# Kernel optimization log

Measured on AMD Instinct MI355X. Metric: run time of the kernel, lower is better.

The kernel has to match this reference:

```python
import jax, jax.numpy as jnp
import numpy as np

B, ISIZE, N, OSIZE = 2048, 512, 2048, 128
TC = 1.0 / 10.0  # dt/tau
PX = 0.5


def setup_inputs() -> dict:
    key = jax.random.key(0)
    ks = jax.random.split(key, 16)
    s = 0.01
    return {
        "x": jax.random.normal(ks[0], (B, ISIZE), jnp.float32),
        "h0_in": jax.random.normal(ks[1], (B, N), jnp.float32),
        "h1_in": jax.random.normal(ks[2], (B, N), jnp.float32),
        "h2_in": jax.random.normal(ks[3], (B, N), jnp.float32),
        "i_to_h0": s * jax.random.normal(ks[4], (ISIZE, N), jnp.float32),
        "h0_w": s * jax.random.normal(ks[5], (N, N), jnp.float32),
        "h0_b": s * jax.random.uniform(ks[6], (N,), jnp.float32),
        "h0_to_h1": s * jax.random.normal(ks[7], (N, N), jnp.float32),
        "h1_w": s * jax.random.normal(ks[8], (N, N), jnp.float32),
        "h1_b": s * jax.random.uniform(ks[9], (N,), jnp.float32),
        "h1_to_h2": s * jax.random.normal(ks[10], (N, N), jnp.float32),
        "h2_w": s * jax.random.normal(ks[11], (N, N), jnp.float32),
        "h2_b": s * jax.random.uniform(ks[12], (N,), jnp.float32),
        "w_out": s * jax.random.normal(ks[13], (N, OSIZE), jnp.float32),
        # Bernoulli(px) sparsity masks (non-trainable buffers in the original)
        "m01": (jax.random.uniform(ks[14], (N, N)) < PX).astype(jnp.float32),
        "m12": (jax.random.uniform(ks[15], (N, N)) < PX).astype(jnp.float32),
    }


def reference(x, h0_in, h1_in, h2_in, i_to_h0, h0_w, h0_b, h0_to_h1,
              h1_w, h1_b, h1_to_h2, h2_w, h2_b, w_out, m01, m12):
    tc = TC
    # zero-diagonal mask applied to every recurrent weight (no self-connections)
    diag = 1.0 - jnp.eye(N, dtype=h0_w.dtype)
    # replicate_ashok=True: feedforward weights are sparsified by Bernoulli masks
    h01 = h0_to_h1 * m01
    h12 = h1_to_h2 * m12

    # layer 0: input drive + masked recurrence + leaky integration
    h0 = h0_in * (1.0 - tc) + jax.nn.relu(
        x @ i_to_h0 + h0_in @ (h0_w * diag) + h0_b) * tc
    # layer 1
    h1 = h1_in * (1.0 - tc) + jax.nn.relu(
        h0 @ h01 + h1_in @ (h1_w * diag) + h1_b) * tc
    # layer 2
    h2 = h2_in * (1.0 - tc) + jax.nn.relu(
        h1 @ h12 + h2_in @ (h2_w * diag) + h2_b) * tc

    out = h2 @ w_out  # Linear without bias (replicate_ashok=True)
    return (h0, h1, h2, out)
```

## Files before the change

kernel.cpp:

```cpp
#include <hip/hip_runtime.h>
#include <hip/hip_bf16.h>
#include <stdint.h>

typedef __bf16 bf16;
typedef __bf16 bf16x8 __attribute__((ext_vector_type(8)));
typedef float f32x4 __attribute__((ext_vector_type(4)));

#define BB   2048
#define ISZ  512
#define NN   2048
#define OSZ  128

struct PackD { const float* src; bf16* dst; int W, ld, off, n8; };
struct TD    { const float* src; const float* msk; bf16* dst;
               int Ncols, ld_dst, k_off, mode, ntx, start; };
struct PAll  { PackD p[4]; TD d[7]; int packBlocks; };

__global__ __launch_bounds__(256) void prep_all_k(PAll a) {
  if ((int)blockIdx.x < a.packBlocks) {
    int idx = blockIdx.x * 256 + threadIdx.x;
    PackD d = a.p[0]; int base = 0;
#pragma unroll
    for (int i = 1; i < 4; ++i) if (idx >= a.p[i - 1].n8) { d = a.p[i]; base = a.p[i - 1].n8; }
    if (idx >= d.n8) return;
    int e = (idx - base) * 8;
    int m = e / d.W;
    int c = e - m * d.W;
    const float4 v0 = *reinterpret_cast<const float4*>(d.src + e);
    const float4 v1 = *reinterpret_cast<const float4*>(d.src + e + 4);
    bf16x8 o;
    o[0] = (bf16)v0.x; o[1] = (bf16)v0.y; o[2] = (bf16)v0.z; o[3] = (bf16)v0.w;
    o[4] = (bf16)v1.x; o[5] = (bf16)v1.y; o[6] = (bf16)v1.z; o[7] = (bf16)v1.w;
    *reinterpret_cast<bf16x8*>(d.dst + (size_t)m * d.ld + d.off + c) = o;
    return;
  }
  int bid = blockIdx.x - a.packBlocks;
  TD d = a.d[0];
#pragma unroll
  for (int i = 1; i < 7; ++i) if (bid >= a.d[i].start) d = a.d[i];
  int local = bid - d.start;
  int k0 = (local % d.ntx) * 32;
  int n0 = (local / d.ntx) * 32;
  __shared__ float t[32][33];
  const int tx = threadIdx.x & 31, ty = threadIdx.x >> 5;
#pragma unroll
  for (int i = 0; i < 4; ++i) {
    int k = k0 + ty + i * 8;
    float v = d.src[(size_t)k * d.Ncols + n0 + tx];
    if (d.mode == 1 && k == (n0 + tx)) v = 0.f;
    if (d.mode == 2) v *= d.msk[(size_t)k * d.Ncols + n0 + tx];
    t[ty + i * 8][tx] = v;
  }
  __syncthreads();
#pragma unroll
  for (int i = 0; i < 4; ++i) {
    int n = n0 + ty + i * 8;
    d.dst[(size_t)n * d.ld_dst + d.k_off + k0 + tx] = (bf16)t[tx][ty + i * 8];
  }
}

struct GP {
  const bf16* A; const bf16* B;
  int K, lda, ldb;
  const float* hin; const float* bias; const float* radd;
  float* outf; int ld_out;
  bf16* nxt; int ld_nxt;
  int epi;
};

__device__ __forceinline__ void gload16(const bf16* g, bf16* l) {
  __builtin_amdgcn_global_load_lds(
      (const __attribute__((address_space(1))) void*)g,
      (__attribute__((address_space(3))) void*)l, 16, 0, 0);
}

__device__ __forceinline__ void epilogue_store(const GP& p, int row, int col, float v) {
  size_t oidx = (size_t)row * p.ld_out + col;
  if (p.epi == 0) {
    float pre = v + p.bias[col];
    if (p.radd) pre += p.radd[oidx];
    float h = p.hin[oidx] * 0.9f + fmaxf(pre, 0.f) * 0.1f;
    p.outf[oidx] = h;
    p.nxt[(size_t)row * p.ld_nxt + col] = (bf16)h;
  } else {
    p.outf[oidx] = v;
  }
}

template<int BM, int BN>
__device__ __forceinline__ void gemm_body8(const GP p) {
  constexpr int BK = 32;
  constexpr int WM = BM / 2, WN = BN / 4;
  constexpr int FM = WM / 16, FN = WN / 16;
  __shared__ bf16 As[2][BM][BK];
  __shared__ bf16 Bs[2][BN][BK];
  const int tid  = threadIdx.x;
  const int lane = tid & 63;
  const int wave = tid >> 6;
  const int gx = gridDim.x, nwg = gx * gridDim.y;
  const int lid = blockIdx.x + gx * blockIdx.y;
  const int q = nwg >> 3;
  const int swz = (lid & 7) * q + (lid >> 3);
  const int m0 = (swz / gx) * BM, n0 = (swz % gx) * BN;
  const int wm0 = (wave >> 2) * WM, wn0 = (wave & 3) * WN;
  const int srow = lane >> 2;
  const int scolE = (((lane & 3) ^ ((lane >> 3) & 3)) * 8);
  const int frow = lane & 15;
  const int rcolE = (((lane >> 4) ^ ((frow >> 1) & 3)) * 8);

  f32x4 acc[FM][FN];
#pragma unroll
  for (int i = 0; i < FM; ++i)
#pragma unroll
    for (int j = 0; j < FN; ++j)
#pragma unroll
      for (int r = 0; r < 4; ++r) acc[i][j][r] = 0.f;

  auto stage = [&](int buf, int t) {
    const int k0 = t * BK;
#pragma unroll
    for (int c = wave; c < BM / 16; c += 8) {
      const bf16* g = p.A + (size_t)(m0 + c * 16 + srow) * p.lda + k0 + scolE;
      gload16(g, &As[buf][0][0] + c * 512);
    }
#pragma unroll
    for (int c = wave; c < BN / 16; c += 8) {
      const bf16* g = p.B + (size_t)(n0 + c * 16 + srow) * p.ldb + k0 + scolE;
      gload16(g, &Bs[buf][0][0] + c * 512);
    }
  };

  const int nt = p.K / BK;
  stage(0, 0);
  __syncthreads();
  int cur = 0;
  for (int t = 0; t < nt; ++t) {
    if (t + 1 < nt) stage(cur ^ 1, t + 1);
    bf16x8 af[FM], bfrag[FN];
#pragma unroll
    for (int i = 0; i < FM; ++i)
      af[i] = *reinterpret_cast<const bf16x8*>(&As[cur][wm0 + i * 16 + frow][rcolE]);
#pragma unroll
    for (int j = 0; j < FN; ++j)
      bfrag[j] = *reinterpret_cast<const bf16x8*>(&Bs[cur][wn0 + j * 16 + frow][rcolE]);
#pragma unroll
    for (int i = 0; i < FM; ++i)
#pragma unroll
      for (int j = 0; j < FN; ++j)
        acc[i][j] = __builtin_amdgcn_mfma_f32_16x16x32_bf16(af[i], bfrag[j], acc[i][j], 0, 0, 0);
    __syncthreads();
    cur ^= 1;
  }

#pragma unroll
  for (int i = 0; i < FM; ++i)
#pragma unroll
    for (int j = 0; j < FN; ++j)
#pragma unroll
      for (int r = 0; r < 4; ++r)
        epilogue_store(p, m0 + wm0 + i * 16 + (lane >> 4) * 4 + r,
                       n0 + wn0 + j * 16 + (lane & 15), acc[i][j][r]);
}

__global__ __launch_bounds__(512) void k_tri(GP p0, GP p1, GP p2) {
  GP p;
  if (blockIdx.z == 0) p = p0;
  else if (blockIdx.z == 1) p = p1;
  else p = p2;
  gemm_body8<128, 128>(p);
}

__global__ __launch_bounds__(512) void k_split(GP p0, GP p1) {
  gemm_body8<128, 128>(blockIdx.z == 0 ? p0 : p1);
}

__global__ __launch_bounds__(512) void k_out(GP p) { gemm_body8<32, 64>(p); }

__global__ __launch_bounds__(256) void k_epi(const float* __restrict__ P0,
                                             const float* __restrict__ P1,
                                             const float* __restrict__ radd,
                                             const float* __restrict__ hin,
                                             const float* __restrict__ bias,
                                             float* __restrict__ outf,
                                             bf16* __restrict__ nxt) {
  int e = (blockIdx.x * 256 + threadIdx.x) * 8;
  int colb = e & (NN - 1);
  const float4 a0 = *reinterpret_cast<const float4*>(P0 + e);
  const float4 a1 = *reinterpret_cast<const float4*>(P0 + e + 4);
  const float4 b0 = *reinterpret_cast<const float4*>(P1 + e);
  const float4 b1 = *reinterpret_cast<const float4*>(P1 + e + 4);
  const float4 r0 = *reinterpret_cast<const float4*>(radd + e);
  const float4 r1 = *reinterpret_cast<const float4*>(radd + e + 4);
  const float4 h0 = *reinterpret_cast<const float4*>(hin + e);
  const float4 h1 = *reinterpret_cast<const float4*>(hin + e + 4);
  const float4 c0 = *reinterpret_cast<const float4*>(bias + colb);
  const float4 c1 = *reinterpret_cast<const float4*>(bias + colb + 4);
  float pa[8] = {a0.x, a0.y, a0.z, a0.w, a1.x, a1.y, a1.z, a1.w};
  float pb[8] = {b0.x, b0.y, b0.z, b0.w, b1.x, b1.y, b1.z, b1.w};
  float pr[8] = {r0.x, r0.y, r0.z, r0.w, r1.x, r1.y, r1.z, r1.w};
  float ph[8] = {h0.x, h0.y, h0.z, h0.w, h1.x, h1.y, h1.z, h1.w};
  float pc[8] = {c0.x, c0.y, c0.z, c0.w, c1.x, c1.y, c1.z, c1.w};
  float4 o0, o1;
  bf16x8 nb;
#pragma unroll
  for (int j = 0; j < 8; ++j) {
    float pre = pa[j] + pb[j] + pr[j] + pc[j];
    float h = ph[j] * 0.9f + fmaxf(pre, 0.f) * 0.1f;
    (j < 4 ? (&o0.x)[j] : (&o1.x)[j - 4]) = h;
    nb[j] = (bf16)h;
  }
  *reinterpret_cast<float4*>(outf + e) = o0;
  *reinterpret_cast<float4*>(outf + e + 4) = o1;
  *reinterpret_cast<bf16x8*>(nxt + e) = nb;
}

extern "C" void kernel_launch(void* const* d_in, const int* in_sizes, int n_in,
                              void* d_out, int out_size, void* d_ws, size_t ws_size,
                              hipStream_t stream) {
  const float* x        = (const float*)d_in[0];
  const float* h0_in    = (const float*)d_in[1];
  const float* h1_in    = (const float*)d_in[2];
  const float* h2_in    = (const float*)d_in[3];
  const float* i_to_h0  = (const float*)d_in[4];
  const float* h0_w     = (const float*)d_in[5];
  const float* h0_b     = (const float*)d_in[6];
  const float* h0_to_h1 = (const float*)d_in[7];
  const float* h1_w     = (const float*)d_in[8];
  const float* h1_b     = (const float*)d_in[9];
  const float* h1_to_h2 = (const float*)d_in[10];
  const float* h2_w     = (const float*)d_in[11];
  const float* h2_b     = (const float*)d_in[12];
  const float* w_out    = (const float*)d_in[13];
  const float* m01      = (const float*)d_in[14];
  const float* m12      = (const float*)d_in[15];
  float* out = (float*)d_out;

  uint8_t* ws = (uint8_t*)d_ws;
  constexpr size_t OFF_A0  = 0;
  constexpr size_t OFF_W0  = OFF_A0 + 10485760;
  constexpr size_t OFF_W1R = OFF_W0 + 10485760;
  constexpr size_t OFF_W2R = OFF_W1R + 8388608;
  constexpr size_t OFF_W01 = OFF_W2R + 8388608;
  constexpr size_t OFF_W12 = OFF_W01 + 8388608;
  constexpr size_t OFF_WO  = OFF_W12 + 8388608;
  constexpr size_t OFF_AR1 = OFF_WO + 524288;
  constexpr size_t OFF_AR2 = OFF_AR1 + 8388608;
  constexpr size_t OFF_AH0 = OFF_AR2 + 8388608;
  constexpr size_t WS_NEED = OFF_AH0 + 8388608;
  if (ws_size < WS_NEED) return;

  bf16* A0  = (bf16*)(ws + OFF_A0);
  bf16* Wt0 = (bf16*)(ws + OFF_W0);
  bf16* W1r = (bf16*)(ws + OFF_W1R);
  bf16* W2r = (bf16*)(ws + OFF_W2R);
  bf16* W01 = (bf16*)(ws + OFF_W01);
  bf16* W12 = (bf16*)(ws + OFF_W12);
  bf16* WtO = (bf16*)(ws + OFF_WO);
  bf16* Ar1 = (bf16*)(ws + OFF_AR1);
  bf16* Ar2 = (bf16*)(ws + OFF_AR2);
  bf16* Ah0 = (bf16*)(ws + OFF_AH0);
  bf16* Ah1 = Ar1;
  bf16* Ah2 = Ar2;
  float* P0 = (float*)(ws + 0);
  float* P1 = (float*)(ws + 16777216);

  float* o_h0  = out;
  float* o_h1  = out + (size_t)BB * NN;
  float* o_h2  = out + (size_t)2 * BB * NN;
  float* o_out = out + (size_t)3 * BB * NN;

  PAll pa;
  int n8a = BB * ISZ / 8;
  int n8b = n8a + BB * NN / 8;
  int n8c = n8b + BB * NN / 8;
  int n8d = n8c + BB * NN / 8;
  pa.p[0] = {x,     A0,  ISZ, ISZ + NN, 0,   n8a};
  pa.p[1] = {h0_in, A0,  NN,  ISZ + NN, ISZ, n8b};
  pa.p[2] = {h1_in, Ar1, NN,  NN,       0,   n8c};
  pa.p[3] = {h2_in, Ar2, NN,  NN,       0,   n8d};
  pa.packBlocks = (n8d + 255) / 256;
  int s0 = 0;
  pa.d[0] = {i_to_h0,  nullptr, Wt0, NN,  ISZ + NN, 0,   0, ISZ / 32, s0}; s0 += (ISZ / 32) * (NN / 32);
  pa.d[1] = {h0_w,     nullptr, Wt0, NN,  ISZ + NN, ISZ, 1, NN / 32,  s0}; s0 += (NN / 32) * (NN / 32);
  pa.d[2] = {h1_w,     nullptr, W1r, NN,  NN,       0,   1, NN / 32,  s0}; s0 += (NN / 32) * (NN / 32);
  pa.d[3] = {h2_w,     nullptr, W2r, NN,  NN,       0,   1, NN / 32,  s0}; s0 += (NN / 32) * (NN / 32);
  pa.d[4] = {h0_to_h1, m01,     W01, NN,  NN,       0,   2, NN / 32,  s0}; s0 += (NN / 32) * (NN / 32);
  pa.d[5] = {h1_to_h2, m12,     W12, NN,  NN,       0,   2, NN / 32,  s0}; s0 += (NN / 32) * (NN / 32);
  pa.d[6] = {w_out,    nullptr, WtO, OSZ, NN,       0,   0, NN / 32,  s0}; s0 += (NN / 32) * (OSZ / 32);
  prep_all_k<<<pa.packBlocks + s0, 256, 0, stream>>>(pa);

  GP pS0{A0,  Wt0, ISZ + NN, ISZ + NN, ISZ + NN, h0_in, h0_b, nullptr,
         o_h0, NN, Ah0, NN, 0};
  GP pR1{Ar1, W1r, NN, NN, NN, nullptr, nullptr, nullptr, o_h1, NN, nullptr, 0, 1};
  GP pR2{Ar2, W2r, NN, NN, NN, nullptr, nullptr, nullptr, o_h2, NN, nullptr, 0, 1};
  k_tri<<<dim3(NN / 128, BB / 128, 3), 512, 0, stream>>>(pS0, pR1, pR2);

  GP pG1a{Ah0,          W01,          NN / 2, NN, NN, nullptr, nullptr, nullptr, P0, NN, nullptr, 0, 1};
  GP pG1b{Ah0 + NN / 2, W01 + NN / 2, NN / 2, NN, NN, nullptr, nullptr, nullptr, P1, NN, nullptr, 0, 1};
  k_split<<<dim3(NN / 128, BB / 128, 2), 512, 0, stream>>>(pG1a, pG1b);
  k_epi<<<BB * NN / 2048, 256, 0, stream>>>(P0, P1, o_h1, h1_in, h1_b, o_h1, Ah1);

  GP pG2a{Ah1,          W12,          NN / 2, NN, NN, nullptr, nullptr, nullptr, P0, NN, nullptr, 0, 1};
  GP pG2b{Ah1 + NN / 2, W12 + NN / 2, NN / 2, NN, NN, nullptr, nullptr, nullptr, P1, NN, nullptr, 0, 1};
  k_split<<<dim3(NN / 128, BB / 128, 2), 512, 0, stream>>>(pG2a, pG2b);
  k_epi<<<BB * NN / 2048, 256, 0, stream>>>(P0, P1, o_h2, h2_in, h2_b, o_h2, Ah2);

  GP pO{Ah2, WtO, NN, NN, NN, nullptr, nullptr, nullptr, o_out, OSZ, nullptr, 0, 1};
  k_out<<<dim3(OSZ / 64, BB / 32), 512, 0, stream>>>(pO);
}
```

Measured before the change: 257.6 us.

## Use intra-block split-K GEMM with BK=64 for the big 128x128 GEMMs

Adds a new GEMM body for the large 128x128 tile kernels. It uses a 64-wide K step and splits the 8 waves into two K-halves that each compute a 64x64 sub-tile per wave, then reduces the two partial accumulators through LDS before the fused epilogue. The aim is to halve the number of barriers per unit of K and raise MFMA work per LDS load, at the cost of more LDS, more registers and an extra reduction step. The small output GEMM loses its grouped tile swizzle and now uses plain block indexing.

```diff
diff --git a/kernel.cpp b/kernel.cpp
--- a/kernel.cpp
+++ b/kernel.cpp
@@ -87,6 +87,103 @@
   }
 }
 
+__device__ __forceinline__ void gemm_ks(const GP p) {
+  __shared__ __align__(16) bf16 sm[2][2][128][64];
+  const int lane = threadIdx.x & 63;
+  const int wave = threadIdx.x >> 6;
+  const int ks = wave >> 2;
+  const int sp = wave & 3;
+  const int gx = gridDim.x, nwg = gx * gridDim.y;
+  const int lid = blockIdx.x + gx * blockIdx.y;
+  const int q = nwg >> 3;
+  const int swz = (lid & 7) * q + (lid >> 3);
+  const int m0 = (swz / gx) * 128, n0 = (swz % gx) * 128;
+  const int wm0 = (sp >> 1) * 64, wn0 = (sp & 1) * 64;
+  const int srow = lane >> 3;
+  const int scol = ((lane & 7) ^ srow) * 8;
+  const int frow = lane & 15;
+  const int rcol = (((ks << 2) + (lane >> 4)) ^ (frow & 7)) * 8;
+
+  f32x4 acc[4][4];
+#pragma unroll
+  for (int i = 0; i < 4; ++i)
+#pragma unroll
+    for (int j = 0; j < 4; ++j)
+#pragma unroll
+      for (int r = 0; r < 4; ++r) acc[i][j][r] = 0.f;
+
+  auto stage = [&](int buf, int t) {
+    const int k0 = t * 64;
+#pragma unroll
+    for (int h = 0; h < 2; ++h) {
+      const int c = wave + h * 8;
+      gload16(p.A + (size_t)(m0 + c * 8 + srow) * p.lda + k0 + scol,
+              &sm[buf][0][0][0] + c * 512);
+      gload16(p.B + (size_t)(n0 + c * 8 + srow) * p.ldb + k0 + scol,
+              &sm[buf][1][0][0] + c * 512);
+    }
+  };
+
+  const int nt = p.K / 64;
+  stage(0, 0);
+  int cur = 0;
+  for (int t = 0; t < nt; ++t) {
+    if (t + 1 < nt) {
+      stage(cur ^ 1, t + 1);
+      asm volatile("s_waitcnt vmcnt(4)" ::: "memory");
+    } else {
+      asm volatile("s_waitcnt vmcnt(0)" ::: "memory");
+    }
+    __builtin_amdgcn_s_barrier();
+
+    bf16x8 af[4], bf_[4];
+#pragma unroll
+    for (int i = 0; i < 4; ++i)
+      af[i] = *reinterpret_cast<const bf16x8*>(&sm[cur][0][wm0 + i * 16 + frow][rcol]);
+#pragma unroll
+    for (int j = 0; j < 4; ++j)
+      bf_[j] = *reinterpret_cast<const bf16x8*>(&sm[cur][1][wn0 + j * 16 + frow][rcol]);
+#pragma unroll
+    for (int i = 0; i < 4; ++i)
+#pragma unroll
+      for (int j = 0; j < 4; ++j)
+        acc[i][j] = __builtin_amdgcn_mfma_f32_16x16x32_bf16(af[i], bf_[j], acc[i][j], 0, 0, 0);
+
+    if (t + 1 < nt) {
+      asm volatile("s_waitcnt lgkmcnt(0)" ::: "memory");
+      __builtin_amdgcn_s_barrier();
+    }
+    cur ^= 1;
+  }
+
+  asm volatile("s_waitcnt lgkmcnt(0)" ::: "memory");
+  __builtin_amdgcn_s_barrier();
+  float* red = (float*)&sm[0][0][0][0];
+  if (ks == 1) {
+#pragma unroll
+    for (int i = 0; i < 4; ++i)
+#pragma unroll
+      for (int j = 0; j < 4; ++j)
+        *reinterpret_cast<f32x4*>(&red[sp * 4096 + (i * 4 + j) * 256 + lane * 4]) = acc[i][j];
+    asm volatile("s_waitcnt lgkmcnt(0)" ::: "memory");
+  }
+  __builtin_amdgcn_s_barrier();
+  if (ks == 0) {
+#pragma unroll
+    for (int i = 0; i < 4; ++i)
+#pragma unroll
+      for (int j = 0; j < 4; ++j) {
+        f32x4 o = *reinterpret_cast<const f32x4*>(&red[sp * 4096 + (i * 4 + j) * 256 + lane * 4]);
+#pragma unroll
+        for (int r = 0; r < 4; ++r) acc[i][j][r] += o[r];
+#pragma unroll
+        for (int r = 0; r < 4; ++r)
+          epilogue_store(p, m0 + wm0 + i * 16 + (lane >> 4) * 4 + r,
+                         n0 + wn0 + j * 16 + (lane & 15), acc[i][j][r]);
+      }
+  }
+}
+
 template<int BM, int BN>
 __device__ __forceinline__ void gemm_body8(const GP p) {
   constexpr int BK = 32;
@@ -94,14 +191,9 @@
   constexpr int FM = WM / 16, FN = WN / 16;
   __shared__ bf16 As[2][BM][BK];
   __shared__ bf16 Bs[2][BN][BK];
-  const int tid  = threadIdx.x;
-  const int lane = tid & 63;
-  const int wave = tid >> 6;
-  const int gx = gridDim.x, nwg = gx * gridDim.y;
-  const int lid = blockIdx.x + gx * blockIdx.y;
-  const int q = nwg >> 3;
-  const int swz = (lid & 7) * q + (lid >> 3);
-  const int m0 = (swz / gx) * BM, n0 = (swz % gx) * BN;
+  const int lane = threadIdx.x & 63;
+  const int wave = threadIdx.x >> 6;
+  const int m0 = blockIdx.y * BM, n0 = blockIdx.x * BN;
   const int wm0 = (wave >> 2) * WM, wn0 = (wave & 3) * WN;
   const int srow = lane >> 2;
   const int scolE = (((lane & 3) ^ ((lane >> 3) & 3)) * 8);
@@ -167,11 +259,11 @@
   if (blockIdx.z == 0) p = p0;
   else if (blockIdx.z == 1) p = p1;
   else p = p2;
-  gemm_body8<128, 128>(p);
+  gemm_ks(p);
 }
 
 __global__ __launch_bounds__(512) void k_split(GP p0, GP p1) {
-  gemm_body8<128, 128>(blockIdx.z == 0 ? p0 : p1);
+  gemm_ks(blockIdx.z == 0 ? p0 : p1);
 }
 
 __global__ __launch_bounds__(512) void k_out(GP p) { gemm_body8<32, 64>(p); }
```

Result: faster. 233.6 us (-9.3%).
